# Optimization experiments

Hardware: AMD Instinct MI355X
Metric: run time of the kernel (lower is better)

The kernel has to match this reference:

```python
import jax, jax.numpy as jnp
import numpy as np

U = 256  # units


def _lstm_scan(x, W, R, bc):
    """Run the custom LSTM over time axis of x [B,T,D].

    W: (D,4U) stacked [ki|kf|ko|kc]; R: (U,4U) stacked [ri|rf|ro|rc]; bc: (U,).
    Faithful quirks: no bias on i/f/o gates; c_new = sigmoid(f*c + i*cand);
    h_new = tanh(c_new) * o.
    Returns (last_h [B,U], outputs [B,T,U]).
    """
    B = x.shape[0]
    xW = jnp.einsum('btd,dg->tbg', x, W)  # precompute input projections, (T,B,4U)

    def step(carry, xw):
        h, c = carry
        g = xw + h @ R  # (B,4U)
        i = jax.nn.sigmoid(g[:, 0 * U:1 * U])
        f = jax.nn.sigmoid(g[:, 1 * U:2 * U])
        o = jax.nn.sigmoid(g[:, 2 * U:3 * U])
        cand = jnp.tanh(g[:, 3 * U:4 * U] + bc)
        c_new = jax.nn.sigmoid(f * c + i * cand)
        h_new = jnp.tanh(c_new) * o
        return (h_new, c_new), h_new

    h0 = jnp.zeros((B, U), dtype=x.dtype)
    c0 = jnp.zeros((B, U), dtype=x.dtype)
    (h_last, _), hs = jax.lax.scan(step, (h0, c0), xW)
    return h_last, jnp.swapaxes(hs, 0, 1)  # (B,T,U)


def setup_inputs() -> dict:
    key = jax.random.key(0)
    ks = jax.random.split(key, 5)
    B, T, D = 16, 2048, 256
    s_in = 1.0 / np.sqrt(D)
    s_rec = 1.0 / np.sqrt(U)
    return {
        'x': jax.random.normal(ks[0], (B, T, D), dtype=jnp.float32),
        'W_f': jax.random.normal(ks[1], (D, 4 * U), dtype=jnp.float32) * s_in,
        'R_f': jax.random.normal(ks[2], (U, 4 * U), dtype=jnp.float32) * s_rec,
        'bc_f': jnp.zeros((U,), dtype=jnp.float32),
        'W_b': jax.random.normal(ks[3], (D, 4 * U), dtype=jnp.float32) * s_in,
        'R_b': jax.random.normal(ks[4], (U, 4 * U), dtype=jnp.float32) * s_rec,
        'bc_b': jnp.zeros((U,), dtype=jnp.float32),
    }


def reference(x, W_f, R_f, bc_f, W_b, R_b, bc_b):
    # forward direction
    _, out_f = _lstm_scan(x, W_f, R_f, bc_f)
    # backward direction: K.rnn(go_backwards=True) iterates reversed inputs and
    # returns outputs in iteration (reversed-time) order, NOT re-reversed.
    _, out_b = _lstm_scan(x[:, ::-1, :], W_b, R_b, bc_b)
    return jnp.concatenate([out_f, out_b], axis=-1)  # (B,T,2U)
```

## Files before the change

kernel.cpp:

```cpp
#include <hip/hip_runtime.h>
#include <hip/hip_bf16.h>
#include <hip/hip_fp16.h>

#define TT 2048
#define BB 16
#define DD 256
#define GG 1024
#define UU 256

using f32x4  = __attribute__((ext_vector_type(4))) float;
using short8 = __attribute__((ext_vector_type(8))) short;
using f16x8  = __attribute__((ext_vector_type(8))) _Float16;
using u32x4  = __attribute__((ext_vector_type(4))) unsigned int;

static __device__ __forceinline__ unsigned short f2h_u(float f){
  _Float16 h = (_Float16)f;
  return __builtin_bit_cast(unsigned short, h);
}
static __device__ __forceinline__ float h2f(unsigned short u){
  return (float)__builtin_bit_cast(_Float16, u);
}
static __device__ __forceinline__ unsigned short f2bf_u(float f){
  __hip_bfloat16 b = __float2bfloat16(f);
  return __builtin_bit_cast(unsigned short, b);
}
static __device__ __forceinline__ float sigmoid_f(float x){
  return 1.0f / (1.0f + __expf(-x));
}
static __device__ __forceinline__ float tanh_f(float x){
  float ax = fabsf(x);
  float e  = __expf(2.0f*ax);
  float r  = 1.0f - 2.0f/(e + 1.0f);
  return copysignf(r, x);
}
static __device__ __forceinline__ f32x4 mfma16x16x32_f16(f16x8 a, f16x8 b, f32x4 c){
  return __builtin_amdgcn_mfma_f32_16x16x32_f16(a, b, c, 0, 0, 0);
}

__global__ __launch_bounds__(256) void cvt_x_kernel(const float* __restrict__ x,
                                                    unsigned short* __restrict__ xh){
  int gid = blockIdx.x*256 + threadIdx.x;
  const float4* xv = (const float4*)x;
  float4 v = xv[gid];
  unsigned int u0 = (unsigned int)f2bf_u(v.x) | ((unsigned int)f2bf_u(v.y) << 16);
  unsigned int u1 = (unsigned int)f2bf_u(v.z) | ((unsigned int)f2bf_u(v.w) << 16);
  ((uint2*)xh)[gid] = make_uint2(u0, u1);
}

__global__ __launch_bounds__(256) void cvt_wt_kernel(const float* __restrict__ Wf,
                                                     const float* __restrict__ Wb,
                                                     unsigned short* __restrict__ wt){
  int gid = blockIdx.x*256 + threadIdx.x;
  int d   = gid >> 18;
  int rem = gid & 262143;
  int n   = rem >> 8;
  int k   = rem & 255;
  const float* src = d ? Wb : Wf;
  wt[gid] = f2bf_u(src[k*GG + n]);
}

__global__ __launch_bounds__(256) void cvt_rt_kernel(const float* __restrict__ Rf,
                                                     const float* __restrict__ Rb,
                                                     unsigned short* __restrict__ rt){
  int gid = blockIdx.x*256 + threadIdx.x;
  int d   = gid >> 18;
  int rem = gid & 262143;
  int c   = rem >> 8;
  int p   = rem & 255;
  int Qb  = c >> 7, tc = c & 127;
  int ul  = tc >> 2, g = tc & 3;
  int ucol = g*256 + Qb*32 + ul;
  int s = p >> 5, l4g = (p >> 3) & 3, e = p & 7;
  int k = 32*s + (e < 4 ? 4*l4g + e : 16 + 4*l4g + (e - 4));
  const float* src = d ? Rb : Rf;
  rt[gid] = f2h_u(src[k*GG + ucol]);
}

__global__ __launch_bounds__(256) void gemm_projT(const unsigned short* __restrict__ Ah,
                                                  const unsigned short* __restrict__ BTh,
                                                  unsigned short* __restrict__ Cd,
                                                  int xstart, int Tc){
  __shared__ __align__(16) unsigned short smem[18432];
  unsigned short* sA = smem;
  unsigned short* sB = smem + 9216;
  unsigned short* sC = smem;

  int mt  = blockIdx.x >> 3;
  int nt  = blockIdx.x & 7;
  int tid = threadIdx.x;

  const unsigned short* Bb = BTh + (size_t)nt*128*DD;

  int w = tid >> 6, lane = tid & 63, l15 = lane & 15, l4 = lane >> 4;
  int wm = w >> 1, wn = w & 1;

  f32x4 zero4 = {0.0f, 0.0f, 0.0f, 0.0f};
  f32x4 acc[4][4];
#pragma unroll
  for (int i = 0; i < 4; ++i)
#pragma unroll
    for (int j = 0; j < 4; ++j) acc[i][j] = zero4;

  for (int kt = 0; kt < 4; ++kt){
    __syncthreads();
#pragma unroll
    for (int i = 0; i < 4; ++i){
      int ch = tid + i*256;
      int r = ch >> 3, c8 = ch & 7;
      int bb = r >> 3, ti = r & 7;
      int tx = xstart + mt*8 + ti;
      *(uint4*)(sA + r*72 + c8*8) = *(const uint4*)(Ah + ((size_t)bb*TT + tx)*DD + kt*64 + c8*8);
      *(uint4*)(sB + r*72 + c8*8) = *(const uint4*)(Bb + (size_t)r*DD + kt*64 + c8*8);
    }
    __syncthreads();
#pragma unroll
    for (int ks = 0; ks < 2; ++ks){
      short8 a[4], b[4];
#pragma unroll
      for (int mf = 0; mf < 4; ++mf)
        a[mf] = *(const short8*)(sA + (wm*64 + mf*16 + l15)*72 + ks*32 + l4*8);
#pragma unroll
      for (int nf = 0; nf < 4; ++nf)
        b[nf] = *(const short8*)(sB + (wn*64 + nf*16 + l15)*72 + ks*32 + l4*8);
#pragma unroll
      for (int mf = 0; mf < 4; ++mf)
#pragma unroll
        for (int nf = 0; nf < 4; ++nf)
          acc[mf][nf] = __builtin_amdgcn_mfma_f32_16x16x32_bf16(a[mf], b[nf], acc[mf][nf], 0, 0, 0);
    }
  }
  __syncthreads();
#pragma unroll
  for (int mf = 0; mf < 4; ++mf)
#pragma unroll
    for (int nf = 0; nf < 4; ++nf)
#pragma unroll
      for (int r = 0; r < 4; ++r)
        sC[(wm*64 + mf*16 + l4*4 + r)*136 + wn*64 + nf*16 + l15] = f2h_u(acc[mf][nf][r]);
  __syncthreads();
  int c = tid >> 1, half = tid & 1;
#pragma unroll
  for (int ti = 0; ti < 8; ++ti){
    unsigned short* slab = Cd + ((size_t)(mt*8 + ti)*GG + nt*128)*16;
    unsigned short v[8];
#pragma unroll
    for (int j = 0; j < 8; ++j)
      v[j] = sC[((half*8 + j)*8 + ti)*136 + c];
    uint4 pk;
    pk.x = (unsigned int)v[0] | ((unsigned int)v[1] << 16);
    pk.y = (unsigned int)v[2] | ((unsigned int)v[3] << 16);
    pk.z = (unsigned int)v[4] | ((unsigned int)v[5] << 16);
    pk.w = (unsigned int)v[6] | ((unsigned int)v[7] << 16);
    *(uint4*)(slab + c*16 + half*8) = pk;
  }
}

template<int Q>
__device__ __forceinline__ void scan_body(
    unsigned short* hT,
    const unsigned short* __restrict__ projT,
    const unsigned short* __restrict__ rt,
    const float* __restrict__ bcf, const float* __restrict__ bcb,
    float* __restrict__ out,
    float* __restrict__ stH, float* __restrict__ stC,
    unsigned short* __restrict__ xchg,
    int* __restrict__ flags,
    int t0, int t1, int Tc, int first, int d)
{
  int tid = threadIdx.x;
  int w = tid >> 6, l = tid & 63, l15 = l & 15, l4 = l >> 4;

  u32x4 frag[8];
  {
    const unsigned short* Rd = rt + (size_t)d*262144
                             + ((size_t)(Q*128 + w*16 + l15))*256 + l4*8;
#pragma unroll
    for (int s = 0; s < 8; ++s)
      frag[s] = *(const u32x4*)(Rd + s*32);
  }
#pragma unroll
  for (int s = 0; s < 8; ++s)
    asm volatile("" : "+v"(frag[s]));

  const float* stHb = stH + d*4096;
  for (int idx = tid; idx < 4096; idx += 512){
    int b = idx >> 8, u = idx & 255;
    hT[(u >> 2)*68 + b*4 + (u & 3)] = first ? (unsigned short)0
                                            : f2h_u(stHb[b*256 + u]);
  }

  const int u_loc = 4*w + l4, u_g = 32*Q + u_loc;
  float c_r = 0.f, h_r = 0.f;
  if (!first) c_r = stC[(d*16 + l15)*256 + u_g];
  float bc_r = (d ? bcb : bcf)[u_g];

  const unsigned short* prj = projT + (size_t)d*Tc*16384;
  const int myflag = (d*8 + Q)*32;
  const int p = (Q + w) & 7;
  const int paflag = (d*8 + p)*32;
  const unsigned long long* xull = (const unsigned long long*)xchg;
  const int Tl = t1 - t0;

  __syncthreads();

  for (int s = 0; s < Tl; ++s){
    int t = t0 + s;
    int ps = d ? (Tl - 1 - s) : s;

    const unsigned short* pr = prj + (size_t)ps*16384;
    unsigned short pj0 = pr[(0*256 + u_g)*16 + l15];
    unsigned short pj1 = pr[(1*256 + u_g)*16 + l15];
    unsigned short pj2 = pr[(2*256 + u_g)*16 + l15];
    unsigned short pj3 = pr[(3*256 + u_g)*16 + l15];

    unsigned long long v0 = 0, v1 = 0;
    if (s > 0 && w >= 1){
      while (__hip_atomic_load(&flags[paflag], __ATOMIC_RELAXED, __HIP_MEMORY_SCOPE_AGENT) < s)
        __builtin_amdgcn_s_sleep(1);
      size_t base = (((size_t)d*2 + ((s - 1) & 1))*8 + p)*128;
      v0 = __hip_atomic_load(&xull[base + 2*l    ], __ATOMIC_RELAXED, __HIP_MEMORY_SCOPE_AGENT);
      v1 = __hip_atomic_load(&xull[base + 2*l + 1], __ATOMIC_RELAXED, __HIP_MEMORY_SCOPE_AGENT);
    }

    f32x4 acc = {0.f, 0.f, 0.f, 0.f};
    {
      uint2 b0 = *(const uint2*)&hT[(Q*8     + l4)*68 + l15*4];
      uint2 b1 = *(const uint2*)&hT[(Q*8 + 4 + l4)*68 + l15*4];
      u32x4 bv = {b0.x, b0.y, b1.x, b1.y};
      acc = mfma16x16x32_f16(__builtin_bit_cast(f16x8, frag[Q]),
                             __builtin_bit_cast(f16x8, bv), acc);
    }

    if (s > 0 && w >= 1){
      int uq = 8*p + (l >> 3), bq = 2*(l & 7);
      *(uint2*)&hT[uq*68 + bq*4    ] = make_uint2((unsigned)v0, (unsigned)(v0 >> 32));
      *(uint2*)&hT[uq*68 + bq*4 + 4] = make_uint2((unsigned)v1, (unsigned)(v1 >> 32));
    }
    __syncthreads();

#pragma unroll
    for (int j = 1; j < 8; ++j){
      const int sg = (Q + j) & 7;
      uint2 b0 = *(const uint2*)&hT[(sg*8     + l4)*68 + l15*4];
      uint2 b1 = *(const uint2*)&hT[(sg*8 + 4 + l4)*68 + l15*4];
      u32x4 bv = {b0.x, b0.y, b1.x, b1.y};
      acc = mfma16x16x32_f16(__builtin_bit_cast(f16x8, frag[sg]),
                             __builtin_bit_cast(f16x8, bv), acc);
    }
    __syncthreads();

    float gi = acc[0] + h2f(pj0);
    float gf = acc[1] + h2f(pj1);
    float go = acc[2] + h2f(pj2);
    float gc = acc[3] + h2f(pj3) + bc_r;
    float ig = sigmoid_f(gi);
    float fg = sigmoid_f(gf);
    float og = sigmoid_f(go);
    float cand = tanh_f(gc);
    c_r = sigmoid_f(fg*c_r + ig*cand);
    float h = tanh_f(c_r) * og;
    h_r = h;

    unsigned short hu = f2h_u(h);
    hT[(8*Q + w)*68 + l15*4 + l4] = hu;
    xchg[((size_t)(d*2 + (s & 1))*8 + Q)*512 + w*64 + l15*4 + l4] = hu;
    asm volatile("s_waitcnt vmcnt(0)" ::: "memory");
    __syncthreads();
    if (tid == 0)
      __hip_atomic_store(&flags[myflag], s + 1, __ATOMIC_RELAXED, __HIP_MEMORY_SCOPE_AGENT);
    out[((size_t)l15*TT + t)*512 + d*256 + u_g] = h;
  }

  stC[(d*16 + l15)*256 + u_g] = c_r;
  stH[(d*16 + l15)*256 + u_g] = h_r;
}

__global__ __attribute__((amdgpu_flat_work_group_size(512, 512), amdgpu_waves_per_eu(2, 2)))
void lstm_scan_mfma(const unsigned short* __restrict__ projT,
                    const unsigned short* __restrict__ rt,
                    const float* __restrict__ bcf, const float* __restrict__ bcb,
                    float* __restrict__ out,
                    float* __restrict__ stH, float* __restrict__ stC,
                    unsigned short* __restrict__ xchg,
                    int* __restrict__ flags,
                    int t0, int t1, int Tc, int first)
{
  __shared__ __align__(16) unsigned short hT[64*68];
  int blk = blockIdx.x;
  int d = blk & 7, Q = blk >> 3;
  if (d >= 2) return;
  switch (Q){
    case 0: scan_body<0>(hT, projT, rt, bcf, bcb, out, stH, stC, xchg, flags, t0, t1, Tc, first, d); break;
    case 1: scan_body<1>(hT, projT, rt, bcf, bcb, out, stH, stC, xchg, flags, t0, t1, Tc, first, d); break;
    case 2: scan_body<2>(hT, projT, rt, bcf, bcb, out, stH, stC, xchg, flags, t0, t1, Tc, first, d); break;
    case 3: scan_body<3>(hT, projT, rt, bcf, bcb, out, stH, stC, xchg, flags, t0, t1, Tc, first, d); break;
    case 4: scan_body<4>(hT, projT, rt, bcf, bcb, out, stH, stC, xchg, flags, t0, t1, Tc, first, d); break;
    case 5: scan_body<5>(hT, projT, rt, bcf, bcb, out, stH, stC, xchg, flags, t0, t1, Tc, first, d); break;
    case 6: scan_body<6>(hT, projT, rt, bcf, bcb, out, stH, stC, xchg, flags, t0, t1, Tc, first, d); break;
    default: scan_body<7>(hT, projT, rt, bcf, bcb, out, stH, stC, xchg, flags, t0, t1, Tc, first, d); break;
  }
}

extern "C" void kernel_launch(void* const* d_in, const int* in_sizes, int n_in,
                              void* d_out, int out_size, void* d_ws, size_t ws_size,
                              hipStream_t stream){
  const float* x   = (const float*)d_in[0];
  const float* Wf  = (const float*)d_in[1];
  const float* Rf  = (const float*)d_in[2];
  const float* bcf = (const float*)d_in[3];
  const float* Wb  = (const float*)d_in[4];
  const float* Rb  = (const float*)d_in[5];
  const float* bcb = (const float*)d_in[6];
  float* out = (float*)d_out;
  char* ws = (char*)d_ws;

  const size_t OFF_XH    = 0;
  const size_t OFF_WT    = 16777216;
  const size_t OFF_RT    = OFF_WT + 1048576;
  const size_t OFF_STH   = OFF_RT + 1048576;
  const size_t OFF_STC   = OFF_STH + 32768;
  const size_t OFF_XCHG  = OFF_STC + 32768;
  const size_t OFF_FLAGS = OFF_XCHG + 32768;
  const size_t OFF_PROJT = OFF_FLAGS + 4096;

  unsigned short* xh    = (unsigned short*)(ws + OFF_XH);
  unsigned short* wt    = (unsigned short*)(ws + OFF_WT);
  unsigned short* rt    = (unsigned short*)(ws + OFF_RT);
  float*          stH   = (float*)(ws + OFF_STH);
  float*          stC   = (float*)(ws + OFF_STC);
  unsigned short* xchg  = (unsigned short*)(ws + OFF_XCHG);
  int*            flags = (int*)(ws + OFF_FLAGS);
  unsigned short* projT = (unsigned short*)(ws + OFF_PROJT);

  int Tc = TT;
  while (Tc > 128 && OFF_PROJT + (size_t)65536*Tc > ws_size) Tc >>= 1;

  cvt_x_kernel<<<8192, 256, 0, stream>>>(x, xh);
  cvt_wt_kernel<<<2048, 256, 0, stream>>>(Wf, Wb, wt);
  cvt_rt_kernel<<<2048, 256, 0, stream>>>(Rf, Rb, rt);

  int nch = TT / Tc;
  for (int ch = 0; ch < nch; ++ch){
    int t0 = ch*Tc, t1 = t0 + Tc;
    gemm_projT<<<Tc, 256, 0, stream>>>(xh, wt,          projT,                     t0,      Tc);
    gemm_projT<<<Tc, 256, 0, stream>>>(xh, wt + 262144, projT + (size_t)Tc*GG*16,  TT - t1, Tc);
    hipMemsetAsync(flags, 0, 2048, stream);
    lstm_scan_mfma<<<64, 512, 0, stream>>>(projT, rt, bcf, bcb, out, stH, stC, xchg, flags,
                                           t0, t1, Tc, ch == 0 ? 1 : 0);
  }
}
```

Measured before the change: 3.806 ms.

## Replace flag-based inter-block handoff with self-validating tagged h exchange

Each exchanged h value is now stored as a 32-bit word that packs the fp16 value with a timestep tag. Consumers poll the data words directly until every tag matches, instead of spinning on a separate per-block flag and then loading the data. This removes the vmcnt wait, one block barrier and the flag store from the producer side, which shortens the serial critical path of each step. In exchange the exchange buffer doubles in size, consumers issue more loads, and correctness now relies on relaxed per-word atomics and a one-time memset of the buffer.

```diff
diff --git a/kernel.cpp b/kernel.cpp
--- a/kernel.cpp
+++ b/kernel.cpp
@@ -163,8 +163,7 @@
     const float* __restrict__ bcf, const float* __restrict__ bcb,
     float* __restrict__ out,
     float* __restrict__ stH, float* __restrict__ stC,
-    unsigned short* __restrict__ xchg,
-    int* __restrict__ flags,
+    unsigned int* __restrict__ xchg,
     int t0, int t1, int Tc, int first, int d)
 {
   int tid = threadIdx.x;
@@ -195,10 +194,9 @@
   float bc_r = (d ? bcb : bcf)[u_g];
 
   const unsigned short* prj = projT + (size_t)d*Tc*16384;
-  const int myflag = (d*8 + Q)*32;
   const int p = (Q + w) & 7;
-  const int paflag = (d*8 + p)*32;
-  const unsigned long long* xull = (const unsigned long long*)xchg;
+  const size_t xib0 = (((size_t)d*2 + 0)*8 + p)*512 + 8u*(unsigned)l;
+  const size_t exb  = ((size_t)d*2*8 + Q)*512 + w*64 + l15*4 + l4;
   const int Tl = t1 - t0;
 
   __syncthreads();
@@ -206,21 +204,21 @@
   for (int s = 0; s < Tl; ++s){
     int t = t0 + s;
     int ps = d ? (Tl - 1 - s) : s;
+
+    unsigned dv[8];
+    const unsigned int* qp = nullptr;
+    if (s > 0 && w >= 1){
+      qp = xchg + xib0 + (size_t)((s - 1) & 1)*4096;
+#pragma unroll
+      for (int k = 0; k < 8; ++k)
+        dv[k] = __hip_atomic_load(qp + k, __ATOMIC_RELAXED, __HIP_MEMORY_SCOPE_AGENT);
+    }
 
     const unsigned short* pr = prj + (size_t)ps*16384;
     unsigned short pj0 = pr[(0*256 + u_g)*16 + l15];
     unsigned short pj1 = pr[(1*256 + u_g)*16 + l15];
     unsigned short pj2 = pr[(2*256 + u_g)*16 + l15];
     unsigned short pj3 = pr[(3*256 + u_g)*16 + l15];
-
-    unsigned long long v0 = 0, v1 = 0;
-    if (s > 0 && w >= 1){
-      while (__hip_atomic_load(&flags[paflag], __ATOMIC_RELAXED, __HIP_MEMORY_SCOPE_AGENT) < s)
-        __builtin_amdgcn_s_sleep(1);
-      size_t base = (((size_t)d*2 + ((s - 1) & 1))*8 + p)*128;
-      v0 = __hip_atomic_load(&xull[base + 2*l    ], __ATOMIC_RELAXED, __HIP_MEMORY_SCOPE_AGENT);
-      v1 = __hip_atomic_load(&xull[base + 2*l + 1], __ATOMIC_RELAXED, __HIP_MEMORY_SCOPE_AGENT);
-    }
 
     f32x4 acc = {0.f, 0.f, 0.f, 0.f};
     {
@@ -232,9 +230,23 @@
     }
 
     if (s > 0 && w >= 1){
-      int uq = 8*p + (l >> 3), bq = 2*(l & 7);
-      *(uint2*)&hT[uq*68 + bq*4    ] = make_uint2((unsigned)v0, (unsigned)(v0 >> 32));
-      *(uint2*)&hT[uq*68 + bq*4 + 4] = make_uint2((unsigned)v1, (unsigned)(v1 >> 32));
+      const unsigned te = (unsigned)(t0 + s);
+      for (;;){
+        bool ok = true;
+#pragma unroll
+        for (int k = 0; k < 8; ++k) ok &= ((dv[k] >> 16) == te);
+        if (ok) break;
+#pragma unroll
+        for (int k = 0; k < 8; ++k)
+          dv[k] = __hip_atomic_load(qp + k, __ATOMIC_RELAXED, __HIP_MEMORY_SCOPE_AGENT);
+      }
+      int uq = 8*p + (l >> 3), bo = 8*(l & 7);
+      uint2 A  = make_uint2((dv[0] & 0xffffu) | ((dv[1] & 0xffffu) << 16),
+                            (dv[2] & 0xffffu) | ((dv[3] & 0xffffu) << 16));
+      uint2 Bv = make_uint2((dv[4] & 0xffffu) | ((dv[5] & 0xffffu) << 16),
+                            (dv[6] & 0xffffu) | ((dv[7] & 0xffffu) << 16));
+      *(uint2*)&hT[uq*68 + bo    ] = A;
+      *(uint2*)&hT[uq*68 + bo + 4] = Bv;
     }
     __syncthreads();
 
@@ -263,12 +275,15 @@
 
     unsigned short hu = f2h_u(h);
     hT[(8*Q + w)*68 + l15*4 + l4] = hu;
-    xchg[((size_t)(d*2 + (s & 1))*8 + Q)*512 + w*64 + l15*4 + l4] = hu;
-    asm volatile("s_waitcnt vmcnt(0)" ::: "memory");
-    __syncthreads();
-    if (tid == 0)
-      __hip_atomic_store(&flags[myflag], s + 1, __ATOMIC_RELAXED, __HIP_MEMORY_SCOPE_AGENT);
+    __hip_atomic_store(&xchg[exb + (size_t)(s & 1)*4096],
+                       (unsigned)hu | ((unsigned)(t0 + s + 1) << 16),
+                       __ATOMIC_RELAXED, __HIP_MEMORY_SCOPE_AGENT);
     out[((size_t)l15*TT + t)*512 + d*256 + u_g] = h;
+
+    __builtin_amdgcn_sched_barrier(0);
+    asm volatile("s_waitcnt lgkmcnt(0)" ::: "memory");
+    __builtin_amdgcn_s_barrier();
+    __builtin_amdgcn_sched_barrier(0);
   }
 
   stC[(d*16 + l15)*256 + u_g] = c_r;
@@ -281,8 +296,7 @@
                     const float* __restrict__ bcf, const float* __restrict__ bcb,
                     float* __restrict__ out,
                     float* __restrict__ stH, float* __restrict__ stC,
-                    unsigned short* __restrict__ xchg,
-                    int* __restrict__ flags,
+                    unsigned int* __restrict__ xchg,
                     int t0, int t1, int Tc, int first)
 {
   __shared__ __align__(16) unsigned short hT[64*68];
@@ -290,14 +304,14 @@
   int d = blk & 7, Q = blk >> 3;
   if (d >= 2) return;
   switch (Q){
-    case 0: scan_body<0>(hT, projT, rt, bcf, bcb, out, stH, stC, xchg, flags, t0, t1, Tc, first, d); break;
-    case 1: scan_body<1>(hT, projT, rt, bcf, bcb, out, stH, stC, xchg, flags, t0, t1, Tc, first, d); break;
-    case 2: scan_body<2>(hT, projT, rt, bcf, bcb, out, stH, stC, xchg, flags, t0, t1, Tc, first, d); break;
-    case 3: scan_body<3>(hT, projT, rt, bcf, bcb, out, stH, stC, xchg, flags, t0, t1, Tc, first, d); break;
-    case 4: scan_body<4>(hT, projT, rt, bcf, bcb, out, stH, stC, xchg, flags, t0, t1, Tc, first, d); break;
-    case 5: scan_body<5>(hT, projT, rt, bcf, bcb, out, stH, stC, xchg, flags, t0, t1, Tc, first, d); break;
-    case 6: scan_body<6>(hT, projT, rt, bcf, bcb, out, stH, stC, xchg, flags, t0, t1, Tc, first, d); break;
-    default: scan_body<7>(hT, projT, rt, bcf, bcb, out, stH, stC, xchg, flags, t0, t1, Tc, first, d); break;
+    case 0: scan_body<0>(hT, projT, rt, bcf, bcb, out, stH, stC, xchg, t0, t1, Tc, first, d); break;
+    case 1: scan_body<1>(hT, projT, rt, bcf, bcb, out, stH, stC, xchg, t0, t1, Tc, first, d); break;
+    case 2: scan_body<2>(hT, projT, rt, bcf, bcb, out, stH, stC, xchg, t0, t1, Tc, first, d); break;
+    case 3: scan_body<3>(hT, projT, rt, bcf, bcb, out, stH, stC, xchg, t0, t1, Tc, first, d); break;
+    case 4: scan_body<4>(hT, projT, rt, bcf, bcb, out, stH, stC, xchg, t0, t1, Tc, first, d); break;
+    case 5: scan_body<5>(hT, projT, rt, bcf, bcb, out, stH, stC, xchg, t0, t1, Tc, first, d); break;
+    case 6: scan_body<6>(hT, projT, rt, bcf, bcb, out, stH, stC, xchg, t0, t1, Tc, first, d); break;
+    default: scan_body<7>(hT, projT, rt, bcf, bcb, out, stH, stC, xchg, t0, t1, Tc, first, d); break;
   }
 }
 
@@ -320,20 +334,20 @@
   const size_t OFF_STH   = OFF_RT + 1048576;
   const size_t OFF_STC   = OFF_STH + 32768;
   const size_t OFF_XCHG  = OFF_STC + 32768;
-  const size_t OFF_FLAGS = OFF_XCHG + 32768;
-  const size_t OFF_PROJT = OFF_FLAGS + 4096;
+  const size_t OFF_PROJT = OFF_XCHG + 131072;
 
   unsigned short* xh    = (unsigned short*)(ws + OFF_XH);
   unsigned short* wt    = (unsigned short*)(ws + OFF_WT);
   unsigned short* rt    = (unsigned short*)(ws + OFF_RT);
   float*          stH   = (float*)(ws + OFF_STH);
   float*          stC   = (float*)(ws + OFF_STC);
-  unsigned short* xchg  = (unsigned short*)(ws + OFF_XCHG);
-  int*            flags = (int*)(ws + OFF_FLAGS);
+  unsigned int*   xchg  = (unsigned int*)(ws + OFF_XCHG);
   unsigned short* projT = (unsigned short*)(ws + OFF_PROJT);
 
   int Tc = TT;
   while (Tc > 128 && OFF_PROJT + (size_t)65536*Tc > ws_size) Tc >>= 1;
+
+  hipMemsetAsync(xchg, 0, 131072, stream);
 
   cvt_x_kernel<<<8192, 256, 0, stream>>>(x, xh);
   cvt_wt_kernel<<<2048, 256, 0, stream>>>(Wf, Wb, wt);
@@ -344,8 +358,7 @@
     int t0 = ch*Tc, t1 = t0 + Tc;
     gemm_projT<<<Tc, 256, 0, stream>>>(xh, wt,          projT,                     t0,      Tc);
     gemm_projT<<<Tc, 256, 0, stream>>>(xh, wt + 262144, projT + (size_t)Tc*GG*16,  TT - t1, Tc);
-    hipMemsetAsync(flags, 0, 2048, stream);
-    lstm_scan_mfma<<<64, 512, 0, stream>>>(projT, rt, bcf, bcb, out, stH, stC, xchg, flags,
+    lstm_scan_mfma<<<64, 512, 0, stream>>>(projT, rt, bcf, bcb, out, stH, stC, xchg,
                                            t0, t1, Tc, ch == 0 ? 1 : 0);
   }
 }
```

Measured after the change: 6.468 ms. +69.9%, slower.
